# Kernel optimization log

Hardware: AMD Instinct MI355X
Metric: run time of the kernel (lower is better)

## Reference

```python
import jax, jax.numpy as jnp
import numpy as np

B, D1, D2, D3 = 4, 64, 64, 64
CIN, COUT = 32, 32
M1, M2, M3 = 8, 8, 8


def setup_inputs() -> dict:
    key = jax.random.key(0)
    k1, k2, k3 = jax.random.split(key, 3)
    x = jax.random.normal(k1, (B, D1, D2, D3, CIN), dtype=jnp.float32)
    # scale ~ random_normal initializer (stddev 0.05 default in keras)
    w_real = jax.random.normal(k2, (CIN, COUT, M1, M2, M3), dtype=jnp.float32) * 0.05
    w_imag = jax.random.normal(k3, (CIN, COUT, M1, M2, M3), dtype=jnp.float32) * 0.05
    return {"x": x, "w_real": w_real, "w_imag": w_imag}


def reference(x, w_real, w_imag):
    # tf.signal.fft3d transforms the innermost 3 dims of [B,D1,D2,D3,C]
    x_ft = jnp.fft.fftn(x.astype(jnp.complex64), axes=(2, 3, 4))
    # low-mode truncation over axes 1,2,3 (as in the original code)
    x_low = x_ft[:, :M1, :M2, :M3, :]                       # [B,M1,M2,M3,CIN]
    w = (w_real + 1j * w_imag).astype(jnp.complex64)         # [CIN,COUT,M1,M2,M3]
    x_low = jnp.transpose(x_low, (0, 4, 1, 2, 3))            # [B,CIN,M1,M2,M3]
    # Faithful to original: i,j of weights are summed out, k is matched.
    out_low = jnp.einsum('bcmnk,coijk->bomnk', x_low, w)     # [B,COUT,M1,M2,M3]
    out_low = jnp.transpose(out_low, (0, 2, 3, 4, 1))        # [B,M1,M2,M3,COUT]
    # zero-padded spectrum (replaces the wasteful tensor_scatter_nd_update)
    out_ft = jnp.zeros((B, D1, D2, D3, COUT), dtype=jnp.complex64)
    out_ft = out_ft.at[:, :M1, :M2, :M3, :].set(out_low)
    y = jnp.fft.ifftn(out_ft, axes=(2, 3, 4))
    return jnp.real(y).astype(jnp.float32)
```

## Files before the change

kernel.cpp:

```cpp
#include <hip/hip_runtime.h>


#define PI2F 6.28318530717958647692f

__device__ __forceinline__ float2 cmul(float2 a, float2 b) {
    return make_float2(a.x * b.x - a.y * b.y, a.x * b.y + a.y * b.x);
}

__global__ void k_weff(const float* __restrict__ wr, const float* __restrict__ wi,
                       float2* __restrict__ Weff) {
    int t = blockIdx.x * 256 + threadIdx.x;
    int base = (t >> 3) * 512 + (t & 7);
    float sr = 0.f, si = 0.f;
    #pragma unroll 8
    for (int ij = 0; ij < 64; ++ij) { sr += wr[base + ij * 8]; si += wi[base + ij * 8]; }
    Weff[t] = make_float2(sr, si);
}

__global__ void k_T(const float2* __restrict__ Weff, float2* __restrict__ T) {
    __shared__ float2 tw32[32];
    __shared__ float2 A[256];
    int t = threadIdx.x;
    int c = blockIdx.x;
    if (t < 32) {
        float s, co_;
        __sincosf((PI2F / 32.f) * (float)t, &s, &co_);
        tw32[t] = make_float2(co_, s);
    }
    __syncthreads();
    {
        float2 acc = make_float2(0.f, 0.f);
        for (int fc = 0; fc < 32; ++fc) {
            float2 v = Weff[fc * 256 + t];
            float2 e = tw32[(fc * c) & 31];
            acc.x += v.x * e.x + v.y * e.y;
            acc.y += v.y * e.x - v.x * e.y;
        }
        A[t] = acc;
    }
    __syncthreads();
    {
        int f3 = t >> 5, co = t & 31;
        float2 acc = make_float2(0.f, 0.f);
        for (int o = 0; o < 32; ++o) {
            float2 v = A[o * 8 + f3];
            float2 e = tw32[(o * co) & 31];
            acc.x += v.x * e.x - v.y * e.y;
            acc.y += v.x * e.y + v.y * e.x;
        }
        T[c * 256 + t] = acc;
    }
}

__global__ void k_dft_d2(const float* __restrict__ x, float2* __restrict__ S1) {
    int t = blockIdx.x * 256 + threadIdx.x;
    int c4 = t & 7;
    int d3 = (t >> 3) & 63;
    int f2 = (t >> 9) & 7;
    int d1 = (t >> 12) & 7;
    int b  = t >> 15;
    const float4* xp = (const float4*)(x + (size_t)b * 8388608 + (size_t)d1 * 131072
                                         + d3 * 32 + c4 * 4);
    float s, c;
    __sincosf((PI2F / 64.f) * (float)f2, &s, &c);
    float2 step = make_float2(c, -s);
    float2 w = make_float2(1.f, 0.f);
    float2 a0 = {0,0}, a1 = {0,0}, a2 = {0,0}, a3 = {0,0};
    for (int d2 = 0; d2 < 64; ++d2) {
        float4 v = xp[d2 * 512];
        a0.x += v.x * w.x; a0.y += v.x * w.y;
        a1.x += v.y * w.x; a1.y += v.y * w.y;
        a2.x += v.z * w.x; a2.y += v.z * w.y;
        a3.x += v.w * w.x; a3.y += v.w * w.y;
        w = cmul(w, step);
    }
    float2* sp = S1 + (size_t)(t >> 9) * 2048 + d3 * 32 + c4 * 4;
    ((float4*)sp)[0] = make_float4(a0.x, a0.y, a1.x, a1.y);
    ((float4*)sp)[1] = make_float4(a2.x, a2.y, a3.x, a3.y);
}

__global__ void k_mid(const float2* __restrict__ S1, const float2* __restrict__ T,
                      float2* __restrict__ S6) {
    __shared__ float2 lin[2048];
    __shared__ float2 ls2[256];
    __shared__ float2 ls5[256];
    __shared__ float2 tw64[64];
    int t = threadIdx.x;
    int gid = blockIdx.x;
    {
        const float4* src = (const float4*)(S1 + (size_t)gid * 2048);
        float4* dst = (float4*)lin;
        #pragma unroll
        for (int j = 0; j < 4; ++j) dst[t + j * 256] = src[t + j * 256];
    }
    if (t < 64) {
        float s, c;
        __sincosf((PI2F / 64.f) * (float)t, &s, &c);
        tw64[t] = make_float2(c, s);
    }
    __syncthreads();
    {
        int f3 = t >> 5, c = t & 31;
        float2 e = tw64[f3];
        float2 step = make_float2(e.x, -e.y);
        float2 w = make_float2(1.f, 0.f);
        float2 acc = make_float2(0.f, 0.f);
        for (int d3 = 0; d3 < 64; ++d3) {
            float2 v = lin[d3 * 32 + c];
            acc.x += v.x * w.x - v.y * w.y;
            acc.y += v.x * w.y + v.y * w.x;
            w = cmul(w, step);
        }
        ls2[f3 * 32 + c] = acc;
    }
    __syncthreads();
    {
        int f3 = t >> 5;
        float2 acc = make_float2(0.f, 0.f);
        for (int c = 0; c < 32; ++c) {
            float2 a = ls2[f3 * 32 + (c)];
            float2 w = T[c * 256 + t];
            acc.x += a.x * w.x - a.y * w.y;
            acc.y += a.x * w.y + a.y * w.x;
        }
        ls5[t] = acc;
    }
    __syncthreads();
    {
        int co = t & 31, d3r = t >> 5;
        float2* outp = S6 + (size_t)gid * 2048;
        #pragma unroll
        for (int j = 0; j < 8; ++j) {
            int d3 = d3r + 8 * j;
            float2 acc = make_float2(0.f, 0.f);
            #pragma unroll
            for (int f3 = 0; f3 < 8; ++f3) {
                float2 v = ls5[f3 * 32 + co];
                float2 e = tw64[(f3 * d3) & 63];
                acc.x += v.x * e.x - v.y * e.y;
                acc.y += v.x * e.y + v.y * e.x;
            }
            outp[d3 * 32 + co] = acc;
        }
    }
}

__global__ void k_final(const float2* __restrict__ S6, float* __restrict__ out) {
    int t4 = blockIdx.x * 256 + threadIdx.x;
    int u = t4 << 2;
    int co = u & 31;
    int d3 = (u >> 5) & 63;
    int d2 = (u >> 11) & 63;
    int d1 = (u >> 17) & 63;
    int b  = u >> 23;
    float4 r;
    if (d1 >= 8) {
        r = make_float4(0.f, 0.f, 0.f, 0.f);
    } else {
        const float2* q = S6 + (size_t)(b * 8 + d1) * 16384 + d3 * 32 + co;
        float a0 = 0.f, a1 = 0.f, a2 = 0.f, a3 = 0.f;
        #pragma unroll
        for (int f2 = 0; f2 < 8; ++f2) {
            float ang = (PI2F / 64.f) * (float)((f2 * d2) & 63);
            float s, c;
            __sincosf(ang, &s, &c);
            float2 v0 = q[f2 * 2048 + 0];
            float2 v1 = q[f2 * 2048 + 1];
            float2 v2 = q[f2 * 2048 + 2];
            float2 v3 = q[f2 * 2048 + 3];
            a0 += v0.x * c - v0.y * s;
            a1 += v1.x * c - v1.y * s;
            a2 += v2.x * c - v2.y * s;
            a3 += v3.x * c - v3.y * s;
        }
        const float sc = 1.f / 131072.f;
        r = make_float4(a0 * sc, a1 * sc, a2 * sc, a3 * sc);
    }
    ((float4*)out)[t4] = r;
}

extern "C" void kernel_launch(void* const* d_in, const int* in_sizes, int n_in,
                              void* d_out, int out_size, void* d_ws, size_t ws_size,
                              hipStream_t stream) {
    const float* x  = (const float*)d_in[0];
    const float* wr = (const float*)d_in[1];
    const float* wi = (const float*)d_in[2];
    float* out = (float*)d_out;

    float2* Weff = (float2*)d_ws;
    float2* T    = Weff + 8192;
    float2* S1   = T + 8192;
    float2* S6   = S1 + 524288;

    k_weff  <<<32,    256, 0, stream>>>(wr, wi, Weff);
    k_T     <<<32,    256, 0, stream>>>(Weff, T);
    k_dft_d2<<<512,   256, 0, stream>>>(x, S1);
    k_mid   <<<256,   256, 0, stream>>>(S1, T, S6);
    k_final <<<32768, 256, 0, stream>>>(S6, out);
}
```

Before: 238.3 us.

## Fuse D2 DFT into forward spectral kernel and tile inverse output via shared memory

The separate D2 DFT kernel is merged into the forward spectral kernel, so each block reads x directly and keeps the intermediate in shared memory. This removes the S1 round trip through global memory and one launch. The final inverse kernel becomes a tiled kernel that stages the S6 slab in shared memory, reads twiddles from a table instead of calling sincos per element, and writes the all-zero d1>=8 region from separate zero-fill blocks. Twiddles in the forward loops now come from table lookups rather than recurrence multiplications. The cost is that only 256 blocks do the large x reduction, which may limit parallelism on that step.

After: 241.7 us. No clear change (+1.4%).

```diff
diff --git a/kernel.cpp b/kernel.cpp
--- a/kernel.cpp
+++ b/kernel.cpp
@@ -2,10 +2,6 @@
 
 
 #define PI2F 6.28318530717958647692f
-
-__device__ __forceinline__ float2 cmul(float2 a, float2 b) {
-    return make_float2(a.x * b.x - a.y * b.y, a.x * b.y + a.y * b.x);
-}
 
 __global__ void k_weff(const float* __restrict__ wr, const float* __restrict__ wi,
                        float2* __restrict__ Weff) {
@@ -52,34 +48,7 @@
     }
 }
 
-__global__ void k_dft_d2(const float* __restrict__ x, float2* __restrict__ S1) {
-    int t = blockIdx.x * 256 + threadIdx.x;
-    int c4 = t & 7;
-    int d3 = (t >> 3) & 63;
-    int f2 = (t >> 9) & 7;
-    int d1 = (t >> 12) & 7;
-    int b  = t >> 15;
-    const float4* xp = (const float4*)(x + (size_t)b * 8388608 + (size_t)d1 * 131072
-                                         + d3 * 32 + c4 * 4);
-    float s, c;
-    __sincosf((PI2F / 64.f) * (float)f2, &s, &c);
-    float2 step = make_float2(c, -s);
-    float2 w = make_float2(1.f, 0.f);
-    float2 a0 = {0,0}, a1 = {0,0}, a2 = {0,0}, a3 = {0,0};
-    for (int d2 = 0; d2 < 64; ++d2) {
-        float4 v = xp[d2 * 512];
-        a0.x += v.x * w.x; a0.y += v.x * w.y;
-        a1.x += v.y * w.x; a1.y += v.y * w.y;
-        a2.x += v.z * w.x; a2.y += v.z * w.y;
-        a3.x += v.w * w.x; a3.y += v.w * w.y;
-        w = cmul(w, step);
-    }
-    float2* sp = S1 + (size_t)(t >> 9) * 2048 + d3 * 32 + c4 * 4;
-    ((float4*)sp)[0] = make_float4(a0.x, a0.y, a1.x, a1.y);
-    ((float4*)sp)[1] = make_float4(a2.x, a2.y, a3.x, a3.y);
-}
-
-__global__ void k_mid(const float2* __restrict__ S1, const float2* __restrict__ T,
+__global__ void k_fwd(const float* __restrict__ x, const float2* __restrict__ T,
                       float2* __restrict__ S6) {
     __shared__ float2 lin[2048];
     __shared__ float2 ls2[256];
@@ -87,12 +56,8 @@
     __shared__ float2 tw64[64];
     int t = threadIdx.x;
     int gid = blockIdx.x;
-    {
-        const float4* src = (const float4*)(S1 + (size_t)gid * 2048);
-        float4* dst = (float4*)lin;
-        #pragma unroll
-        for (int j = 0; j < 4; ++j) dst[t + j * 256] = src[t + j * 256];
-    }
+    int f2 = gid >> 5;
+    int bd1 = gid & 31;
     if (t < 64) {
         float s, c;
         __sincosf((PI2F / 64.f) * (float)t, &s, &c);
@@ -100,25 +65,52 @@
     }
     __syncthreads();
     {
+        int b = bd1 >> 3, d1 = bd1 & 7;
+        const float4* xp = (const float4*)(x + (size_t)b * 8388608 + (size_t)d1 * 131072);
+        int d3a = t >> 3,        c4a = t & 7;
+        int d3b = (t + 256) >> 3, c4b = t & 7;
+        const float4* xa = xp + d3a * 8 + c4a;
+        const float4* xb = xp + d3b * 8 + c4b;
+        float2 A0{0,0}, A1{0,0}, A2{0,0}, A3{0,0};
+        float2 B0{0,0}, B1{0,0}, B2{0,0}, B3{0,0};
+        #pragma unroll 4
+        for (int d2 = 0; d2 < 64; ++d2) {
+            float2 e = tw64[(f2 * d2) & 63];
+            float4 va = xa[d2 * 512];
+            float4 vb = xb[d2 * 512];
+            A0.x += va.x * e.x; A0.y -= va.x * e.y;
+            A1.x += va.y * e.x; A1.y -= va.y * e.y;
+            A2.x += va.z * e.x; A2.y -= va.z * e.y;
+            A3.x += va.w * e.x; A3.y -= va.w * e.y;
+            B0.x += vb.x * e.x; B0.y -= vb.x * e.y;
+            B1.x += vb.y * e.x; B1.y -= vb.y * e.y;
+            B2.x += vb.z * e.x; B2.y -= vb.z * e.y;
+            B3.x += vb.w * e.x; B3.y -= vb.w * e.y;
+        }
+        float4* lp = (float4*)lin;
+        lp[d3a * 16 + c4a * 2]     = make_float4(A0.x, A0.y, A1.x, A1.y);
+        lp[d3a * 16 + c4a * 2 + 1] = make_float4(A2.x, A2.y, A3.x, A3.y);
+        lp[d3b * 16 + c4b * 2]     = make_float4(B0.x, B0.y, B1.x, B1.y);
+        lp[d3b * 16 + c4b * 2 + 1] = make_float4(B2.x, B2.y, B3.x, B3.y);
+    }
+    __syncthreads();
+    {
         int f3 = t >> 5, c = t & 31;
-        float2 e = tw64[f3];
-        float2 step = make_float2(e.x, -e.y);
-        float2 w = make_float2(1.f, 0.f);
         float2 acc = make_float2(0.f, 0.f);
         for (int d3 = 0; d3 < 64; ++d3) {
             float2 v = lin[d3 * 32 + c];
-            acc.x += v.x * w.x - v.y * w.y;
-            acc.y += v.x * w.y + v.y * w.x;
-            w = cmul(w, step);
-        }
-        ls2[f3 * 32 + c] = acc;
+            float2 e = tw64[(f3 * d3) & 63];
+            acc.x += v.x * e.x + v.y * e.y;
+            acc.y += v.y * e.x - v.x * e.y;
+        }
+        ls2[t] = acc;
     }
     __syncthreads();
     {
         int f3 = t >> 5;
         float2 acc = make_float2(0.f, 0.f);
         for (int c = 0; c < 32; ++c) {
-            float2 a = ls2[f3 * 32 + (c)];
+            float2 a = ls2[f3 * 32 + c];
             float2 w = T[c * 256 + t];
             acc.x += a.x * w.x - a.y * w.y;
             acc.y += a.x * w.y + a.y * w.x;
@@ -128,7 +120,7 @@
     __syncthreads();
     {
         int co = t & 31, d3r = t >> 5;
-        float2* outp = S6 + (size_t)gid * 2048;
+        float2* outp = S6 + (size_t)(bd1 * 8 + f2) * 2048;
         #pragma unroll
         for (int j = 0; j < 8; ++j) {
             int d3 = d3r + 8 * j;
@@ -145,38 +137,65 @@
     }
 }
 
-__global__ void k_final(const float2* __restrict__ S6, float* __restrict__ out) {
-    int t4 = blockIdx.x * 256 + threadIdx.x;
-    int u = t4 << 2;
-    int co = u & 31;
-    int d3 = (u >> 5) & 63;
-    int d2 = (u >> 11) & 63;
-    int d1 = (u >> 17) & 63;
-    int b  = u >> 23;
-    float4 r;
-    if (d1 >= 8) {
-        r = make_float4(0.f, 0.f, 0.f, 0.f);
-    } else {
-        const float2* q = S6 + (size_t)(b * 8 + d1) * 16384 + d3 * 32 + co;
+__global__ void k_out(const float2* __restrict__ S6, float* __restrict__ out) {
+    __shared__ float2 slab[8][16][32];
+    __shared__ float2 tw64[64];
+    int t = threadIdx.x;
+    int b = blockIdx.y;
+    int xb = blockIdx.x;
+    if (xb >= 256) {
+        int z = xb - 256;
+        float4* op = (float4*)out + (size_t)b * 2097152 + 262144 + (size_t)z * 2048;
+        float4 zero = make_float4(0.f, 0.f, 0.f, 0.f);
+        #pragma unroll
+        for (int i = 0; i < 8; ++i) op[i * 256 + t] = zero;
+        return;
+    }
+    int d2g = xb >> 5, d1 = (xb >> 2) & 7, d3q = xb & 3;
+    int bd1 = b * 8 + d1;
+    if (t < 64) {
+        float s, c;
+        __sincosf((PI2F / 64.f) * (float)t, &s, &c);
+        tw64[t] = make_float2(c, s);
+    }
+    {
+        const float4* src = (const float4*)S6 + (size_t)bd1 * 8192 + d3q * 256;
+        float4* dst = (float4*)slab;
+        #pragma unroll
+        for (int i = 0; i < 8; ++i) {
+            int f4l = t + 256 * i;
+            int f2 = f4l >> 8, rem = f4l & 255;
+            dst[f4l] = src[f2 * 1024 + rem];
+        }
+    }
+    __syncthreads();
+    int co4 = t & 7, d2l = (t >> 3) & 7, d3r = t >> 6;
+    int d2 = d2g * 8 + d2l;
+    float twr[8], twi[8];
+    #pragma unroll
+    for (int f2 = 0; f2 < 8; ++f2) {
+        float2 e = tw64[(f2 * d2) & 63];
+        twr[f2] = e.x; twi[f2] = e.y;
+    }
+    const float sc = 1.f / 131072.f;
+    float4* op = (float4*)out + ((size_t)(b * 64 + d1) * 64 + d2) * 512;
+    #pragma unroll
+    for (int k = 0; k < 4; ++k) {
+        int d3l = d3r * 4 + k;
+        int d3 = d3q * 16 + d3l;
         float a0 = 0.f, a1 = 0.f, a2 = 0.f, a3 = 0.f;
         #pragma unroll
         for (int f2 = 0; f2 < 8; ++f2) {
-            float ang = (PI2F / 64.f) * (float)((f2 * d2) & 63);
-            float s, c;
-            __sincosf(ang, &s, &c);
-            float2 v0 = q[f2 * 2048 + 0];
-            float2 v1 = q[f2 * 2048 + 1];
-            float2 v2 = q[f2 * 2048 + 2];
-            float2 v3 = q[f2 * 2048 + 3];
-            a0 += v0.x * c - v0.y * s;
-            a1 += v1.x * c - v1.y * s;
-            a2 += v2.x * c - v2.y * s;
-            a3 += v3.x * c - v3.y * s;
-        }
-        const float sc = 1.f / 131072.f;
-        r = make_float4(a0 * sc, a1 * sc, a2 * sc, a3 * sc);
-    }
-    ((float4*)out)[t4] = r;
+            const float4* sp = (const float4*)&slab[f2][d3l][co4 * 4];
+            float4 v01 = sp[0];
+            float4 v23 = sp[1];
+            a0 += v01.x * twr[f2] - v01.y * twi[f2];
+            a1 += v01.z * twr[f2] - v01.w * twi[f2];
+            a2 += v23.x * twr[f2] - v23.y * twi[f2];
+            a3 += v23.z * twr[f2] - v23.w * twi[f2];
+        }
+        op[d3 * 8 + co4] = make_float4(a0 * sc, a1 * sc, a2 * sc, a3 * sc);
+    }
 }
 
 extern "C" void kernel_launch(void* const* d_in, const int* in_sizes, int n_in,
@@ -189,12 +208,10 @@
 
     float2* Weff = (float2*)d_ws;
     float2* T    = Weff + 8192;
-    float2* S1   = T + 8192;
-    float2* S6   = S1 + 524288;
-
-    k_weff  <<<32,    256, 0, stream>>>(wr, wi, Weff);
-    k_T     <<<32,    256, 0, stream>>>(Weff, T);
-    k_dft_d2<<<512,   256, 0, stream>>>(x, S1);
-    k_mid   <<<256,   256, 0, stream>>>(S1, T, S6);
-    k_final <<<32768, 256, 0, stream>>>(S6, out);
-}
+    float2* S6   = T + 8192;
+
+    k_weff<<<32,  256, 0, stream>>>(wr, wi, Weff);
+    k_T   <<<32,  256, 0, stream>>>(Weff, T);
+    k_fwd <<<256, 256, 0, stream>>>(x, T, S6);
+    k_out <<<dim3(1152, 4), 256, 0, stream>>>(S6, out);
+}
```
